# Kernel tuning notes

Hardware: AMD Instinct MI355X
Metric: run time of the kernel (lower is better)

Reference implementation:

```python
import jax, jax.numpy as jnp
import numpy as np

TOP_K = 2


def setup_inputs() -> dict:
    key = jax.random.key(0)
    k1, k2, k3, k4, k5 = jax.random.split(key, 5)
    B, S, D, E, F = 2, 1024, 2048, 8, 768
    scale_in = 1.0 / np.sqrt(D)
    scale_ff = 1.0 / np.sqrt(F)
    return {
        "x": jax.random.normal(k1, (B, S, D), dtype=jnp.float32),
        "w_gate_router": jax.random.normal(k2, (E, D), dtype=jnp.float32) * scale_in,
        "w_gate_proj": jax.random.normal(k3, (E, F, D), dtype=jnp.float32) * scale_in,
        "w_up_proj": jax.random.normal(k4, (E, F, D), dtype=jnp.float32) * scale_in,
        "w_down_proj": jax.random.normal(k5, (E, D, F), dtype=jnp.float32) * scale_ff,
    }


def moe_forward(x, w_gate_router, w_gate_proj, w_up_proj, w_down_proj):
    E = w_gate_router.shape[0]
    # Router: scores [B,S,E], top-k selection, softmax over the k selected scores.
    scores = jnp.einsum("bsd,ed->bse", x, w_gate_router)
    topk_scores, topk_idx = jax.lax.top_k(scores, TOP_K)          # [B,S,K]
    topk_probs = jax.nn.softmax(topk_scores, axis=-1)             # [B,S,K]
    # Dense combine weights: zero for unselected experts (== scatter of topk_probs).
    weights = jnp.sum(topk_probs[..., None] * jax.nn.one_hot(topk_idx, E, dtype=x.dtype), axis=-2)  # [B,S,E]
    # Per-expert SwiGLU computed densely over all tokens (same math as
    # gather/dispatch-per-expert followed by scatter-add combine).
    gate = jnp.einsum("bsd,efd->bsef", x, w_gate_proj)            # [B,S,E,F]
    up = jnp.einsum("bsd,efd->bsef", x, w_up_proj)
    hidden = jax.nn.silu(gate) * up                                # [B,S,E,F]
    # Weighted combine: sum_e weights[b,s,e] * (hidden @ w_down[e].T)
    out = jnp.einsum("bsef,edf,bse->bsd", hidden, w_down_proj, weights)
    return out


def reference(x, w_gate_router, w_gate_proj, w_up_proj, w_down_proj):
    return moe_forward(x, w_gate_router, w_gate_proj, w_up_proj, w_down_proj)
```

## Files before the change

kernel.cpp:

```cpp
#include <hip/hip_runtime.h>

#define T_TOK 2048
#define DIM   2048
#define NEXP  8
#define FF    768
#define NGRP  16
#define BK    64

typedef unsigned short u16;
typedef unsigned int   u32;
typedef __bf16 bf16x8 __attribute__((ext_vector_type(8)));
typedef float  f32x4  __attribute__((ext_vector_type(4)));
typedef u16    u16x4  __attribute__((ext_vector_type(4)));
typedef u16    u16x8  __attribute__((ext_vector_type(8)));

#define AS1 __attribute__((address_space(1)))
#define AS3 __attribute__((address_space(3)))

__device__ __forceinline__ u16 f2bf(float f) {
    union { u32 i; float f; } v; v.f = f;
    u32 r = v.i + 0x7FFF + ((v.i >> 16) & 1);
    return (u16)(r >> 16);
}
__device__ __forceinline__ float bf2f(u16 u) {
    union { u32 i; float f; } v; v.i = ((u32)u) << 16; return v.f;
}

__device__ __forceinline__ void gload16(const u16* g, u16* l) {
    __builtin_amdgcn_global_load_lds((const AS1 u32*)g, (AS3 u32*)l, 16, 0, 0);
}

__global__ void cvt3_kernel(const float* __restrict__ s0, u16* __restrict__ d0,
                            const float* __restrict__ s1, u16* __restrict__ d1,
                            const float* __restrict__ s2, u16* __restrict__ d2) {
    const float* __restrict__ s; u16* __restrict__ d;
    switch (blockIdx.y) {
        case 0: s = s0; d = d0; break;
        case 1: s = s1; d = d1; break;
        default: s = s2; d = d2; break;
    }
    const size_t st = 1536u * 256u;
    size_t t = (size_t)blockIdx.x * 256 + threadIdx.x;
#pragma unroll
    for (int it = 0; it < 4; it++) {
        size_t i = t + (size_t)it * st;
        f32x4 a = ((const f32x4*)s)[i * 2];
        f32x4 b = ((const f32x4*)s)[i * 2 + 1];
        u16x8 o;
#pragma unroll
        for (int j = 0; j < 4; j++) { o[j] = f2bf(a[j]); o[4 + j] = f2bf(b[j]); }
        ((u16x8*)d)[i] = o;
    }
}

__global__ void router_kernel(const float* __restrict__ x, const float* __restrict__ wr,
                              int* cnt, int* rt_e, float* rt_p, u16* __restrict__ xb) {
    int wave = threadIdx.x >> 6, lane = threadIdx.x & 63;
    int t = blockIdx.x * 4 + wave;
    float xv[32];
#pragma unroll
    for (int i = 0; i < 32; i++) xv[i] = x[(size_t)t * DIM + i * 64 + lane];
#pragma unroll
    for (int i = 0; i < 32; i++) xb[(size_t)t * DIM + i * 64 + lane] = f2bf(xv[i]);
    float s[NEXP];
#pragma unroll
    for (int e = 0; e < NEXP; e++) {
        float acc = 0.f;
#pragma unroll
        for (int i = 0; i < 32; i++) acc += xv[i] * wr[(size_t)e * DIM + i * 64 + lane];
        for (int off = 32; off; off >>= 1) acc += __shfl_xor(acc, off);
        s[e] = acc;
    }
    if (lane == 0) {
        int bi = 0; float bv = s[0];
        for (int e = 1; e < NEXP; e++) if (s[e] > bv) { bv = s[e]; bi = e; }
        float sv = -1e30f; int si = 0;
        for (int e = 0; e < NEXP; e++) { if (e == bi) continue; if (s[e] > sv) { sv = s[e]; si = e; } }
        float p0 = 1.f / (1.f + __expf(sv - bv));
        float p1 = 1.f - p0;
        rt_e[t * 2 + 0] = bi; rt_e[t * 2 + 1] = si;
        rt_p[t * 2 + 0] = p0; rt_p[t * 2 + 1] = p1;
        atomicAdd(&cnt[bi * 2 + 0], 1);
        atomicAdd(&cnt[si * 2 + 1], 1);
    }
}

__global__ void scanassign_kernel(const int* cnt, const int* rt_e, const float* rt_p,
                                  int* base_g, int* tile_g, int* tile_m0, int* ntiles,
                                  int* rowtok, float* rowprob) {
    __shared__ int s_base[NGRP];
    __shared__ int s_pos[NGRP];
    int tid = threadIdx.x;
    if (tid < NGRP) s_pos[tid] = 0;
    if (tid < 64) {
        int lane = tid;
        int c = (lane < NGRP) ? cnt[lane] : 0;
        int nt_g = (c + 127) >> 7;
        int pre = 0, tpre = 0;
        for (int i = 0; i < NGRP; i++) {
            int ci = __shfl(c, i), ti = __shfl(nt_g, i);
            if (i < lane) { pre += ci; tpre += ti; }
        }
        if (lane < NGRP) {
            s_base[lane] = pre; base_g[lane] = pre;
            for (int j = 0; j < nt_g; j++) { tile_g[tpre + j] = lane; tile_m0[tpre + j] = j * 128; }
            if (lane == NGRP - 1) *ntiles = tpre + nt_g;
        }
    }
    __syncthreads();
    for (int t = tid; t < T_TOK; t += 256) {
#pragma unroll
        for (int k = 0; k < 2; k++) {
            int g = rt_e[t * 2 + k] * 2 + k;
            int pos = atomicAdd(&s_pos[g], 1);
            int row = s_base[g] + pos;
            rowtok[row] = t;
            rowprob[row] = rt_p[t * 2 + k];
        }
    }
}

__launch_bounds__(256)
__global__ void gateup_kernel(const u16* __restrict__ xb, const u16* __restrict__ wgb,
                              const u16* __restrict__ wub,
                              const int* cnt, const int* base, const int* tile_g,
                              const int* tile_m0, const int* ntiles,
                              const int* rowtok, const float* rowprob,
                              u16* __restrict__ hidden) {
    int tile = blockIdx.x;
    if (tile >= *ntiles) return;
    int g = tile_g[tile], m0 = tile_m0[tile];
    int e = g >> 1;
    int f0 = blockIdx.y * 64;
    int cg = cnt[g], bg_ = base[g];

    __shared__ u16 As[2][128 * BK];
    __shared__ u16 Bs[2][128 * BK];
    __shared__ int   tks[128];
    __shared__ float ps[128];

    int tid = threadIdx.x;
    if (tid < 128) {
        int valid = (m0 + tid) < cg;
        tks[tid] = valid ? rowtok[bg_ + m0 + tid] : 0;
        ps[tid]  = valid ? rowprob[bg_ + m0 + tid] : 0.f;
    }
    __syncthreads();

    int wave = tid >> 6, lane = tid & 63;
    int quad = lane >> 4, l16 = lane & 15;
    int wr = wave >> 1, wc = wave & 1;

    int r8  = lane >> 3;
    int csw = ((lane & 7) ^ r8) * 8;

    const u16* gA[4]; int lA[4];
#pragma unroll
    for (int gi = 0; gi < 4; gi++) {
        int row = wave * 32 + gi * 8 + r8;
        gA[gi] = xb + (size_t)tks[row] * DIM + csw;
        lA[gi] = (wave * 32 + gi * 8) * BK;
    }
    const u16* bsrc = (wave >> 1) ? wub : wgb;
    int fo = (wave & 1) * 8 + r8;
    const u16* gB[4]; int lB[4];
#pragma unroll
    for (int gi = 0; gi < 4; gi++) {
        gB[gi] = bsrc + ((size_t)e * FF + f0 + gi * 16 + fo) * DIM + csw;
        lB[gi] = (gi * 32 + wave * 8) * BK;
    }

    f32x4 acc[4][4] = {};

#pragma unroll
    for (int gi = 0; gi < 4; gi++) gload16(gA[gi], &As[0][0] + lA[gi]);
#pragma unroll
    for (int gi = 0; gi < 4; gi++) gload16(gB[gi], &Bs[0][0] + lB[gi]);
    __syncthreads();

    int sw0 = ((0 * 4 + quad) ^ (l16 & 7)) * 8;
    int sw1 = ((1 * 4 + quad) ^ (l16 & 7)) * 8;

#pragma unroll 2
    for (int kt = 0; kt < DIM / BK; kt++) {
        int cur = kt & 1;
        int kk = (kt + 1) * BK;
        if (kk < DIM) {
#pragma unroll
            for (int gi = 0; gi < 4; gi++) gload16(gA[gi] + kk, &As[cur ^ 1][0] + lA[gi]);
#pragma unroll
            for (int gi = 0; gi < 4; gi++) gload16(gB[gi] + kk, &Bs[cur ^ 1][0] + lB[gi]);
        }
#pragma unroll
        for (int ks = 0; ks < 2; ks++) {
            int sw = ks ? sw1 : sw0;
            bf16x8 a[4], b[4];
#pragma unroll
            for (int mi = 0; mi < 4; mi++)
                a[mi] = *(const bf16x8*)&As[cur][(wr * 64 + mi * 16 + l16) * BK + sw];
#pragma unroll
            for (int ni = 0; ni < 4; ni++)
                b[ni] = *(const bf16x8*)&Bs[cur][(wc * 64 + ni * 16 + l16) * BK + sw];
#pragma unroll
            for (int mi = 0; mi < 4; mi++)
#pragma unroll
                for (int ni = 0; ni < 4; ni++)
                    acc[mi][ni] = __builtin_amdgcn_mfma_f32_16x16x32_bf16(a[mi], b[ni], acc[mi][ni], 0, 0, 0);
        }
        __syncthreads();
    }

    int fb = f0 + wc * 32 + l16;
#pragma unroll
    for (int mi = 0; mi < 4; mi++) {
#pragma unroll
        for (int r = 0; r < 4; r++) {
            int m = wr * 64 + mi * 16 + quad * 4 + r;
            if (m0 + m < cg) {
                float p = ps[m];
                float g0 = acc[mi][0][r], u0 = acc[mi][1][r];
                float g1 = acc[mi][2][r], u1 = acc[mi][3][r];
                size_t rowo = (size_t)(bg_ + m0 + m) * FF;
                hidden[rowo + fb]      = f2bf((g0 / (1.f + __expf(-g0))) * u0 * p);
                hidden[rowo + fb + 16] = f2bf((g1 / (1.f + __expf(-g1))) * u1 * p);
            }
        }
    }
}

__launch_bounds__(256)
__global__ void down_kernel(const u16* __restrict__ hid, const u16* __restrict__ wdb,
                            const int* cnt, const int* base, const int* tile_g,
                            const int* tile_m0, const int* ntiles, const int* rowtok,
                            u16* __restrict__ out0, u16* __restrict__ out1) {
    int tile = blockIdx.x;
    if (tile >= *ntiles) return;
    int g = tile_g[tile], m0 = tile_m0[tile];
    int e = g >> 1, slot = g & 1;
    int d0 = blockIdx.y * 128;
    int cg = cnt[g], bg_ = base[g];

    __shared__ u16 As[2][128 * BK];
    __shared__ u16 Bs[2][128 * BK];
    __shared__ int tks[128];

    int tid = threadIdx.x;
    if (tid < 128) tks[tid] = ((m0 + tid) < cg) ? rowtok[bg_ + m0 + tid] : 0;
    __syncthreads();

    int wave = tid >> 6, lane = tid & 63;
    int quad = lane >> 4, l16 = lane & 15;
    int wr = wave >> 1, wc = wave & 1;

    int r8  = lane >> 3;
    int csw = ((lane & 7) ^ r8) * 8;

    const u16* gA[4]; int lA[4];
#pragma unroll
    for (int gi = 0; gi < 4; gi++) {
        int row = wave * 32 + gi * 8 + r8;
        gA[gi] = hid + (size_t)(bg_ + m0 + row) * FF + csw;
        lA[gi] = (wave * 32 + gi * 8) * BK;
    }
    const u16* gB[4]; int lB[4];
#pragma unroll
    for (int gi = 0; gi < 4; gi++) {
        int n = gi * 32 + wave * 8 + r8;
        gB[gi] = wdb + ((size_t)e * DIM + d0 + n) * FF + csw;
        lB[gi] = (gi * 32 + wave * 8) * BK;
    }

    f32x4 acc[4][4] = {};

#pragma unroll
    for (int gi = 0; gi < 4; gi++) gload16(gA[gi], &As[0][0] + lA[gi]);
#pragma unroll
    for (int gi = 0; gi < 4; gi++) gload16(gB[gi], &Bs[0][0] + lB[gi]);
    __syncthreads();

    int sw0 = ((0 * 4 + quad) ^ (l16 & 7)) * 8;
    int sw1 = ((1 * 4 + quad) ^ (l16 & 7)) * 8;

#pragma unroll 2
    for (int kt = 0; kt < FF / BK; kt++) {
        int cur = kt & 1;
        int kk = (kt + 1) * BK;
        if (kk < FF) {
#pragma unroll
            for (int gi = 0; gi < 4; gi++) gload16(gA[gi] + kk, &As[cur ^ 1][0] + lA[gi]);
#pragma unroll
            for (int gi = 0; gi < 4; gi++) gload16(gB[gi] + kk, &Bs[cur ^ 1][0] + lB[gi]);
        }
#pragma unroll
        for (int ks = 0; ks < 2; ks++) {
            int sw = ks ? sw1 : sw0;
            bf16x8 a[4], b[4];
#pragma unroll
            for (int mi = 0; mi < 4; mi++)
                a[mi] = *(const bf16x8*)&As[cur][(wr * 64 + mi * 16 + l16) * BK + sw];
#pragma unroll
            for (int ni = 0; ni < 4; ni++)
                b[ni] = *(const bf16x8*)&Bs[cur][(wc * 64 + ni * 16 + l16) * BK + sw];
#pragma unroll
            for (int mi = 0; mi < 4; mi++)
#pragma unroll
                for (int ni = 0; ni < 4; ni++)
                    acc[mi][ni] = __builtin_amdgcn_mfma_f32_16x16x32_bf16(a[mi], b[ni], acc[mi][ni], 0, 0, 0);
        }
        __syncthreads();
    }

    u16* outp = slot ? out1 : out0;
#pragma unroll
    for (int mi = 0; mi < 4; mi++) {
#pragma unroll
        for (int ni = 0; ni < 4; ni++) {
            int d = d0 + wc * 64 + ni * 16 + l16;
#pragma unroll
            for (int r = 0; r < 4; r++) {
                int m = wr * 64 + mi * 16 + quad * 4 + r;
                if (m0 + m < cg) {
                    outp[(size_t)tks[m] * DIM + d] = f2bf(acc[mi][ni][r]);
                }
            }
        }
    }
}

__global__ void combine_kernel(const u16* __restrict__ o0, const u16* __restrict__ o1,
                               float* __restrict__ out) {
    int i = blockIdx.x * blockDim.x + threadIdx.x;
    u16x8 a = *(const u16x8*)(o0 + (size_t)i * 8);
    u16x8 b = *(const u16x8*)(o1 + (size_t)i * 8);
    f32x4 r0, r1;
#pragma unroll
    for (int j = 0; j < 4; j++) {
        r0[j] = bf2f(a[j]) + bf2f(b[j]);
        r1[j] = bf2f(a[4 + j]) + bf2f(b[4 + j]);
    }
    *(f32x4*)(out + (size_t)i * 8) = r0;
    *(f32x4*)(out + (size_t)i * 8 + 4) = r1;
}

extern "C" void kernel_launch(void* const* d_in, const int* in_sizes, int n_in,
                              void* d_out, int out_size, void* d_ws, size_t ws_size,
                              hipStream_t stream) {
    const float* x  = (const float*)d_in[0];
    const float* wr = (const float*)d_in[1];
    const float* wg = (const float*)d_in[2];
    const float* wu = (const float*)d_in[3];
    const float* wd = (const float*)d_in[4];
    float* out = (float*)d_out;

    char* W = (char*)d_ws;
    int*   cnt     = (int*)(W + 0);
    int*   base    = (int*)(W + 128);
    int*   ntiles  = (int*)(W + 192);
    int*   tile_g  = (int*)(W + 256);
    int*   tile_m0 = (int*)(W + 512);
    int*   rt_e    = (int*)(W + 1024);
    float* rt_p    = (float*)(W + 20480);
    int*   rowtok  = (int*)(W + 40960);
    float* rowprob = (float*)(W + 61440);
    u16*   hidden  = (u16*)(W + 81920);
    u16*   xb      = (u16*)(W + ((size_t)8  << 20));
    u16*   wgb     = (u16*)(W + ((size_t)17 << 20));
    u16*   wub     = (u16*)(W + ((size_t)43 << 20));
    u16*   wdb     = (u16*)(W + ((size_t)69 << 20));
    u16*   out0    = (u16*)(W + ((size_t)17 << 20));
    u16*   out1    = (u16*)(W + ((size_t)26 << 20));

    hipMemsetAsync(W, 0, 256, stream);

    cvt3_kernel<<<dim3(1536, 3), 256, 0, stream>>>(wg, wgb, wu, wub, wd, wdb);

    router_kernel<<<T_TOK / 4, 256, 0, stream>>>(x, wr, cnt, rt_e, rt_p, xb);
    scanassign_kernel<<<1, 256, 0, stream>>>(cnt, rt_e, rt_p, base, tile_g, tile_m0,
                                             ntiles, rowtok, rowprob);

    gateup_kernel<<<dim3(48, 12), 256, 0, stream>>>(xb, wgb, wub, cnt, base, tile_g, tile_m0,
                                                    ntiles, rowtok, rowprob, hidden);
    down_kernel<<<dim3(48, 16), 256, 0, stream>>>(hidden, wdb, cnt, base, tile_g, tile_m0,
                                                  ntiles, rowtok, out0, out1);
    combine_kernel<<<T_TOK * DIM / (256 * 8), 256, 0, stream>>>(out0, out1, out);
}
```

Baseline: 378.3 us.

## Halve K tile, flatten weight conversion, fuse combine via fp32 atomics

The change drops BK from 64 to 32 in both grouped GEMMs and reworks the LDS swizzle and load mapping to match. The B-tile assignment in the gate/up kernel changes so each wave loads both gate and up rows. It also removes the per-slot bf16 output buffers and the combine kernel: down_kernel now atomically adds fp32 results into the zeroed output, which removes one pass over memory but adds a memset and atomic traffic. The weight conversion kernel is relaunched with four times as many blocks, each converting one vector instead of looping over four.

```diff
diff --git a/kernel.cpp b/kernel.cpp
--- a/kernel.cpp
+++ b/kernel.cpp
@@ -5,7 +5,7 @@
 #define NEXP  8
 #define FF    768
 #define NGRP  16
-#define BK    64
+#define BK    32
 
 typedef unsigned short u16;
 typedef unsigned int   u32;
@@ -39,18 +39,13 @@
         case 1: s = s1; d = d1; break;
         default: s = s2; d = d2; break;
     }
-    const size_t st = 1536u * 256u;
-    size_t t = (size_t)blockIdx.x * 256 + threadIdx.x;
-#pragma unroll
-    for (int it = 0; it < 4; it++) {
-        size_t i = t + (size_t)it * st;
-        f32x4 a = ((const f32x4*)s)[i * 2];
-        f32x4 b = ((const f32x4*)s)[i * 2 + 1];
-        u16x8 o;
-#pragma unroll
-        for (int j = 0; j < 4; j++) { o[j] = f2bf(a[j]); o[4 + j] = f2bf(b[j]); }
-        ((u16x8*)d)[i] = o;
-    }
+    size_t i = (size_t)blockIdx.x * 256 + threadIdx.x;
+    f32x4 a = ((const f32x4*)s)[i * 2];
+    f32x4 b = ((const f32x4*)s)[i * 2 + 1];
+    u16x8 o;
+#pragma unroll
+    for (int j = 0; j < 4; j++) { o[j] = f2bf(a[j]); o[4 + j] = f2bf(b[j]); }
+    ((u16x8*)d)[i] = o;
 }
 
 __global__ void router_kernel(const float* __restrict__ x, const float* __restrict__ wr,
@@ -151,66 +146,62 @@
     int quad = lane >> 4, l16 = lane & 15;
     int wr = wave >> 1, wc = wave & 1;
 
-    int r8  = lane >> 3;
-    int csw = ((lane & 7) ^ r8) * 8;
-
-    const u16* gA[4]; int lA[4];
-#pragma unroll
-    for (int gi = 0; gi < 4; gi++) {
-        int row = wave * 32 + gi * 8 + r8;
+    int r4  = lane >> 2;
+    int csw = ((lane & 3) ^ ((r4 >> 1) & 3)) * 8;
+
+    const u16* gA[2]; int lA[2];
+#pragma unroll
+    for (int gi = 0; gi < 2; gi++) {
+        int row = wave * 32 + gi * 16 + r4;
         gA[gi] = xb + (size_t)tks[row] * DIM + csw;
-        lA[gi] = (wave * 32 + gi * 8) * BK;
-    }
-    const u16* bsrc = (wave >> 1) ? wub : wgb;
-    int fo = (wave & 1) * 8 + r8;
-    const u16* gB[4]; int lB[4];
-#pragma unroll
-    for (int gi = 0; gi < 4; gi++) {
-        gB[gi] = bsrc + ((size_t)e * FF + f0 + gi * 16 + fo) * DIM + csw;
-        lB[gi] = (gi * 32 + wave * 8) * BK;
-    }
+        lA[gi] = (wave * 32 + gi * 16) * BK;
+    }
+    const u16* gB[2]; int lB[2];
+#pragma unroll
+    for (int gi = 0; gi < 2; gi++) {
+        const u16* bsrc = gi ? wub : wgb;
+        gB[gi] = bsrc + ((size_t)e * FF + f0 + wave * 16 + r4) * DIM + csw;
+        lB[gi] = (wave * 32 + gi * 16) * BK;
+    }
+
+    int swz = (quad ^ ((l16 >> 1) & 3)) * 8;
+    int aoff[4], boff[4];
+#pragma unroll
+    for (int mi = 0; mi < 4; mi++) aoff[mi] = (wr * 64 + mi * 16 + l16) * BK + swz;
+#pragma unroll
+    for (int ni = 0; ni < 4; ni++) boff[ni] = (wc * 64 + ni * 16 + l16) * BK + swz;
 
     f32x4 acc[4][4] = {};
 
 #pragma unroll
-    for (int gi = 0; gi < 4; gi++) gload16(gA[gi], &As[0][0] + lA[gi]);
-#pragma unroll
-    for (int gi = 0; gi < 4; gi++) gload16(gB[gi], &Bs[0][0] + lB[gi]);
-    __syncthreads();
-
-    int sw0 = ((0 * 4 + quad) ^ (l16 & 7)) * 8;
-    int sw1 = ((1 * 4 + quad) ^ (l16 & 7)) * 8;
-
-#pragma unroll 2
+    for (int gi = 0; gi < 2; gi++) gload16(gA[gi], &As[0][0] + lA[gi]);
+#pragma unroll
+    for (int gi = 0; gi < 2; gi++) gload16(gB[gi], &Bs[0][0] + lB[gi]);
+    __syncthreads();
+
+    int cur = 0;
     for (int kt = 0; kt < DIM / BK; kt++) {
-        int cur = kt & 1;
         int kk = (kt + 1) * BK;
         if (kk < DIM) {
 #pragma unroll
-            for (int gi = 0; gi < 4; gi++) gload16(gA[gi] + kk, &As[cur ^ 1][0] + lA[gi]);
-#pragma unroll
-            for (int gi = 0; gi < 4; gi++) gload16(gB[gi] + kk, &Bs[cur ^ 1][0] + lB[gi]);
-        }
-#pragma unroll
-        for (int ks = 0; ks < 2; ks++) {
-            int sw = ks ? sw1 : sw0;
-            bf16x8 a[4], b[4];
-#pragma unroll
-            for (int mi = 0; mi < 4; mi++)
-                a[mi] = *(const bf16x8*)&As[cur][(wr * 64 + mi * 16 + l16) * BK + sw];
+            for (int gi = 0; gi < 2; gi++) gload16(gA[gi] + kk, &As[cur ^ 1][0] + lA[gi]);
+#pragma unroll
+            for (int gi = 0; gi < 2; gi++) gload16(gB[gi] + kk, &Bs[cur ^ 1][0] + lB[gi]);
+        }
+        bf16x8 a[4], b[4];
+#pragma unroll
+        for (int mi = 0; mi < 4; mi++) a[mi] = *(const bf16x8*)&As[cur][aoff[mi]];
+#pragma unroll
+        for (int ni = 0; ni < 4; ni++) b[ni] = *(const bf16x8*)&Bs[cur][boff[ni]];
+#pragma unroll
+        for (int mi = 0; mi < 4; mi++)
 #pragma unroll
             for (int ni = 0; ni < 4; ni++)
-                b[ni] = *(const bf16x8*)&Bs[cur][(wc * 64 + ni * 16 + l16) * BK + sw];
-#pragma unroll
-            for (int mi = 0; mi < 4; mi++)
-#pragma unroll
-                for (int ni = 0; ni < 4; ni++)
-                    acc[mi][ni] = __builtin_amdgcn_mfma_f32_16x16x32_bf16(a[mi], b[ni], acc[mi][ni], 0, 0, 0);
-        }
+                acc[mi][ni] = __builtin_amdgcn_mfma_f32_16x16x32_bf16(a[mi], b[ni], acc[mi][ni], 0, 0, 0);
         __syncthreads();
-    }
-
-    int fb = f0 + wc * 32 + l16;
+        cur ^= 1;
+    }
+
 #pragma unroll
     for (int mi = 0; mi < 4; mi++) {
 #pragma unroll
@@ -220,9 +211,9 @@
                 float p = ps[m];
                 float g0 = acc[mi][0][r], u0 = acc[mi][1][r];
                 float g1 = acc[mi][2][r], u1 = acc[mi][3][r];
-                size_t rowo = (size_t)(bg_ + m0 + m) * FF;
-                hidden[rowo + fb]      = f2bf((g0 / (1.f + __expf(-g0))) * u0 * p);
-                hidden[rowo + fb + 16] = f2bf((g1 / (1.f + __expf(-g1))) * u1 * p);
+                size_t rowo = (size_t)(bg_ + m0 + m) * FF + f0 + wc * 32 + l16;
+                hidden[rowo]      = f2bf((g0 / (1.f + __expf(-g0))) * u0 * p);
+                hidden[rowo + 16] = f2bf((g1 / (1.f + __expf(-g1))) * u1 * p);
             }
         }
     }
@@ -232,11 +223,11 @@
 __global__ void down_kernel(const u16* __restrict__ hid, const u16* __restrict__ wdb,
                             const int* cnt, const int* base, const int* tile_g,
                             const int* tile_m0, const int* ntiles, const int* rowtok,
-                            u16* __restrict__ out0, u16* __restrict__ out1) {
+                            float* __restrict__ out) {
     int tile = blockIdx.x;
     if (tile >= *ntiles) return;
     int g = tile_g[tile], m0 = tile_m0[tile];
-    int e = g >> 1, slot = g & 1;
+    int e = g >> 1;
     int d0 = blockIdx.y * 128;
     int cg = cnt[g], bg_ = base[g];
 
@@ -252,65 +243,62 @@
     int quad = lane >> 4, l16 = lane & 15;
     int wr = wave >> 1, wc = wave & 1;
 
-    int r8  = lane >> 3;
-    int csw = ((lane & 7) ^ r8) * 8;
-
-    const u16* gA[4]; int lA[4];
-#pragma unroll
-    for (int gi = 0; gi < 4; gi++) {
-        int row = wave * 32 + gi * 8 + r8;
+    int r4  = lane >> 2;
+    int csw = ((lane & 3) ^ ((r4 >> 1) & 3)) * 8;
+
+    const u16* gA[2]; int lA[2];
+#pragma unroll
+    for (int gi = 0; gi < 2; gi++) {
+        int row = wave * 32 + gi * 16 + r4;
         gA[gi] = hid + (size_t)(bg_ + m0 + row) * FF + csw;
-        lA[gi] = (wave * 32 + gi * 8) * BK;
-    }
-    const u16* gB[4]; int lB[4];
-#pragma unroll
-    for (int gi = 0; gi < 4; gi++) {
-        int n = gi * 32 + wave * 8 + r8;
+        lA[gi] = (wave * 32 + gi * 16) * BK;
+    }
+    const u16* gB[2]; int lB[2];
+#pragma unroll
+    for (int gi = 0; gi < 2; gi++) {
+        int n = wave * 32 + gi * 16 + r4;
         gB[gi] = wdb + ((size_t)e * DIM + d0 + n) * FF + csw;
-        lB[gi] = (gi * 32 + wave * 8) * BK;
-    }
+        lB[gi] = (wave * 32 + gi * 16) * BK;
+    }
+
+    int swz = (quad ^ ((l16 >> 1) & 3)) * 8;
+    int aoff[4], boff[4];
+#pragma unroll
+    for (int mi = 0; mi < 4; mi++) aoff[mi] = (wr * 64 + mi * 16 + l16) * BK + swz;
+#pragma unroll
+    for (int ni = 0; ni < 4; ni++) boff[ni] = (wc * 64 + ni * 16 + l16) * BK + swz;
 
     f32x4 acc[4][4] = {};
 
 #pragma unroll
-    for (int gi = 0; gi < 4; gi++) gload16(gA[gi], &As[0][0] + lA[gi]);
-#pragma unroll
-    for (int gi = 0; gi < 4; gi++) gload16(gB[gi], &Bs[0][0] + lB[gi]);
-    __syncthreads();
-
-    int sw0 = ((0 * 4 + quad) ^ (l16 & 7)) * 8;
-    int sw1 = ((1 * 4 + quad) ^ (l16 & 7)) * 8;
-
-#pragma unroll 2
+    for (int gi = 0; gi < 2; gi++) gload16(gA[gi], &As[0][0] + lA[gi]);
+#pragma unroll
+    for (int gi = 0; gi < 2; gi++) gload16(gB[gi], &Bs[0][0] + lB[gi]);
+    __syncthreads();
+
+    int cur = 0;
     for (int kt = 0; kt < FF / BK; kt++) {
-        int cur = kt & 1;
         int kk = (kt + 1) * BK;
         if (kk < FF) {
 #pragma unroll
-            for (int gi = 0; gi < 4; gi++) gload16(gA[gi] + kk, &As[cur ^ 1][0] + lA[gi]);
-#pragma unroll
-            for (int gi = 0; gi < 4; gi++) gload16(gB[gi] + kk, &Bs[cur ^ 1][0] + lB[gi]);
-        }
-#pragma unroll
-        for (int ks = 0; ks < 2; ks++) {
-            int sw = ks ? sw1 : sw0;
-            bf16x8 a[4], b[4];
-#pragma unroll
-            for (int mi = 0; mi < 4; mi++)
-                a[mi] = *(const bf16x8*)&As[cur][(wr * 64 + mi * 16 + l16) * BK + sw];
+            for (int gi = 0; gi < 2; gi++) gload16(gA[gi] + kk, &As[cur ^ 1][0] + lA[gi]);
+#pragma unroll
+            for (int gi = 0; gi < 2; gi++) gload16(gB[gi] + kk, &Bs[cur ^ 1][0] + lB[gi]);
+        }
+        bf16x8 a[4], b[4];
+#pragma unroll
+        for (int mi = 0; mi < 4; mi++) a[mi] = *(const bf16x8*)&As[cur][aoff[mi]];
+#pragma unroll
+        for (int ni = 0; ni < 4; ni++) b[ni] = *(const bf16x8*)&Bs[cur][boff[ni]];
+#pragma unroll
+        for (int mi = 0; mi < 4; mi++)
 #pragma unroll
             for (int ni = 0; ni < 4; ni++)
-                b[ni] = *(const bf16x8*)&Bs[cur][(wc * 64 + ni * 16 + l16) * BK + sw];
-#pragma unroll
-            for (int mi = 0; mi < 4; mi++)
-#pragma unroll
-                for (int ni = 0; ni < 4; ni++)
-                    acc[mi][ni] = __builtin_amdgcn_mfma_f32_16x16x32_bf16(a[mi], b[ni], acc[mi][ni], 0, 0, 0);
-        }
+                acc[mi][ni] = __builtin_amdgcn_mfma_f32_16x16x32_bf16(a[mi], b[ni], acc[mi][ni], 0, 0, 0);
         __syncthreads();
-    }
-
-    u16* outp = slot ? out1 : out0;
+        cur ^= 1;
+    }
+
 #pragma unroll
     for (int mi = 0; mi < 4; mi++) {
 #pragma unroll
@@ -320,26 +308,11 @@
             for (int r = 0; r < 4; r++) {
                 int m = wr * 64 + mi * 16 + quad * 4 + r;
                 if (m0 + m < cg) {
-                    outp[(size_t)tks[m] * DIM + d] = f2bf(acc[mi][ni][r]);
+                    atomicAdd(&out[(size_t)tks[m] * DIM + d], acc[mi][ni][r]);
                 }
             }
         }
     }
-}
-
-__global__ void combine_kernel(const u16* __restrict__ o0, const u16* __restrict__ o1,
-                               float* __restrict__ out) {
-    int i = blockIdx.x * blockDim.x + threadIdx.x;
-    u16x8 a = *(const u16x8*)(o0 + (size_t)i * 8);
-    u16x8 b = *(const u16x8*)(o1 + (size_t)i * 8);
-    f32x4 r0, r1;
-#pragma unroll
-    for (int j = 0; j < 4; j++) {
-        r0[j] = bf2f(a[j]) + bf2f(b[j]);
-        r1[j] = bf2f(a[4 + j]) + bf2f(b[4 + j]);
-    }
-    *(f32x4*)(out + (size_t)i * 8) = r0;
-    *(f32x4*)(out + (size_t)i * 8 + 4) = r1;
 }
 
 extern "C" void kernel_launch(void* const* d_in, const int* in_sizes, int n_in,
@@ -367,12 +340,11 @@
     u16*   wgb     = (u16*)(W + ((size_t)17 << 20));
     u16*   wub     = (u16*)(W + ((size_t)43 << 20));
     u16*   wdb     = (u16*)(W + ((size_t)69 << 20));
-    u16*   out0    = (u16*)(W + ((size_t)17 << 20));
-    u16*   out1    = (u16*)(W + ((size_t)26 << 20));
 
     hipMemsetAsync(W, 0, 256, stream);
-
-    cvt3_kernel<<<dim3(1536, 3), 256, 0, stream>>>(wg, wgb, wu, wub, wd, wdb);
+    hipMemsetAsync(out, 0, (size_t)T_TOK * DIM * sizeof(float), stream);
+
+    cvt3_kernel<<<dim3(6144, 3), 256, 0, stream>>>(wg, wgb, wu, wub, wd, wdb);
 
     router_kernel<<<T_TOK / 4, 256, 0, stream>>>(x, wr, cnt, rt_e, rt_p, xb);
     scanassign_kernel<<<1, 256, 0, stream>>>(cnt, rt_e, rt_p, base, tile_g, tile_m0,
@@ -381,6 +353,5 @@
     gateup_kernel<<<dim3(48, 12), 256, 0, stream>>>(xb, wgb, wub, cnt, base, tile_g, tile_m0,
                                                     ntiles, rowtok, rowprob, hidden);
     down_kernel<<<dim3(48, 16), 256, 0, stream>>>(hidden, wdb, cnt, base, tile_g, tile_m0,
-                                                  ntiles, rowtok, out0, out1);
-    combine_kernel<<<T_TOK * DIM / (256 * 8), 256, 0, stream>>>(out0, out1, out);
-}
+                                                  ntiles, rowtok, out);
+}
```

New measurement: 364.2 us. 1.04x faster.
